# Optimization experiments

Measured on AMD Instinct MI355X. Metric: run time of the kernel, lower is better.

The kernel has to match this reference:

```python
import jax, jax.numpy as jnp
import numpy as np

NUM_ITEMS = 50000
NUM_USERS = 16384   # static number of user segments (total_user universe)
H0 = 512            # encoder_hidden_size[0]
LAT = 256           # bottleneck (encoder_hidden_size[-1] / decoder_hidden_size[0])
N = 262144          # observed interactions
NT = 262144         # target interactions


def setup_inputs() -> dict:
    key = jax.random.key(0)
    ks = jax.random.split(key, 14)

    def glorot(k, shape):
        fan_in, fan_out = shape[1], shape[0]
        lim = np.sqrt(6.0 / (fan_in + fan_out)).astype(np.float32)
        return jax.random.uniform(k, shape, jnp.float32, -lim, lim)

    return {
        "user": jax.random.randint(ks[0], (N,), 0, NUM_USERS, jnp.int32),
        "item": jax.random.randint(ks[1], (N,), 0, NUM_ITEMS, jnp.int32),
        "rating": jax.random.normal(ks[2], (N,), jnp.float32),
        "target_user": jax.random.randint(ks[3], (NT,), 0, NUM_USERS, jnp.int32),
        "target_item": jax.random.randint(ks[4], (NT,), 0, NUM_ITEMS, jnp.int32),
        "target_rating": jax.random.normal(ks[5], (NT,), jnp.float32),
        # encoder_linear: Linear(num_items, H0)
        "W_enc": glorot(ks[6], (H0, NUM_ITEMS)),
        "b_enc": jnp.zeros((H0,), jnp.float32),
        # Encoder: Linear(H0, LAT) + Tanh
        "W1": glorot(ks[7], (LAT, H0)),
        "b1": jnp.zeros((LAT,), jnp.float32),
        # Decoder: Linear(LAT, H0) + Tanh
        "W2": glorot(ks[8], (H0, LAT)),
        "b2": jnp.zeros((H0,), jnp.float32),
        # decoder_linear: Linear(H0, num_items)
        "W_dec": glorot(ks[9], (NUM_ITEMS, H0)),
        "b_dec": jnp.zeros((NUM_ITEMS,), jnp.float32),
    }


def reference(user, item, rating, target_user, target_item, target_rating,
              W_enc, b_enc, W1, b1, W2, b2, W_dec, b_dec):
    # --- encoder: gather item weight rows, scale by rating, segment-sum per user ---
    # rows: [N, H0] gather from W_enc.T ([NUM_ITEMS, H0])
    rows = W_enc.T[item] * rating[:, None]
    # per-user aggregation over the full user universe (equivalent to the
    # torch unique/sort/index_add path: users with no interactions get 0 -> tanh(bias))
    agg = jax.ops.segment_sum(rows, user, num_segments=NUM_USERS)  # [U, H0]
    x = jnp.tanh(agg + b_enc)
    # --- small dense tanh MLP encoder/decoder ---
    encoded = jnp.tanh(x @ W1.T + b1)          # [U, LAT]
    decoded = jnp.tanh(encoded @ W2.T + b2)    # [U, H0] (dropout = identity, eval mode)
    # --- decoder: gather user codes & item decoder rows, rowwise dot ---
    g = decoded[target_user]                   # [NT, H0]
    w = W_dec[target_item]                     # [NT, H0]
    pred = jnp.sum(g * w, axis=-1) + b_dec[target_item]  # [NT]
    loss = jnp.mean((pred - target_rating) ** 2)
    return pred, loss
```

## Files before the change

### kernel.cpp

```cpp
#include <hip/hip_runtime.h>
#include <hip/hip_bf16.h>
#include <math.h>

#define NUM_ITEMS 50000
#define NUM_USERS 16384
#define H0 512
#define LAT 256
#define FP8_SCALE 64.0f
#define FP8_INV (1.0f / 64.0f)

typedef __attribute__((ext_vector_type(8))) short short8;
typedef __attribute__((ext_vector_type(4))) float floatx4;
typedef __attribute__((ext_vector_type(2))) float vf2;

__device__ __forceinline__ unsigned short f2bf(float f) {
    union { float f; unsigned i; } u; u.f = f;
    unsigned r = u.i + 0x7fff + ((u.i >> 16) & 1);
    return (unsigned short)(r >> 16);
}
__device__ __forceinline__ float bfhi(unsigned v) {
    union { unsigned i; float f; } u; u.i = v & 0xffff0000u; return u.f;
}
__device__ __forceinline__ float bflo(unsigned v) {
    union { unsigned i; float f; } u; u.i = v << 16; return u.f;
}
__device__ __forceinline__ uint4 pack8(const float* v) {
    uint4 p;
    p.x = (unsigned)f2bf(v[0]) | ((unsigned)f2bf(v[1]) << 16);
    p.y = (unsigned)f2bf(v[2]) | ((unsigned)f2bf(v[3]) << 16);
    p.z = (unsigned)f2bf(v[4]) | ((unsigned)f2bf(v[5]) << 16);
    p.w = (unsigned)f2bf(v[6]) | ((unsigned)f2bf(v[7]) << 16);
    return p;
}
__device__ __forceinline__ unsigned pkfp8_4(float a, float b, float c, float d) {
    int v = __builtin_amdgcn_cvt_pk_fp8_f32(a, b, 0, false);
    v = __builtin_amdgcn_cvt_pk_fp8_f32(c, d, v, true);
    return (unsigned)v;
}
__device__ __forceinline__ void fp8x4_to_f32(unsigned v, float* o) {
    vf2 lo = __builtin_amdgcn_cvt_pk_f32_fp8((int)v, false);
    vf2 hi = __builtin_amdgcn_cvt_pk_f32_fp8((int)v, true);
    o[0] = lo.x; o[1] = lo.y; o[2] = hi.x; o[3] = hi.y;
}
__device__ __forceinline__ void unpbf8(uint4 q, float* o) {
    o[0] = bflo(q.x); o[1] = bfhi(q.x);
    o[2] = bflo(q.y); o[3] = bfhi(q.y);
    o[4] = bflo(q.z); o[5] = bfhi(q.z);
    o[6] = bflo(q.w); o[7] = bfhi(q.w);
}

__global__ __launch_bounds__(256) void count_kernel(const int* __restrict__ user, int* __restrict__ cntU,
                                                    const int* __restrict__ t_user, int* __restrict__ cntTU,
                                                    int n, int nt) {
    int i = (blockIdx.x * blockDim.x + threadIdx.x) * 4;
    if (i + 3 < n) {
        int4 u = *(const int4*)(user + i);
        atomicAdd(&cntU[u.x], 1); atomicAdd(&cntU[u.y], 1);
        atomicAdd(&cntU[u.z], 1); atomicAdd(&cntU[u.w], 1);
    } else {
        for (int k = i; k < n; ++k) atomicAdd(&cntU[user[k]], 1);
    }
    if (i + 3 < nt) {
        int4 t = *(const int4*)(t_user + i);
        atomicAdd(&cntTU[t.x], 1); atomicAdd(&cntTU[t.y], 1);
        atomicAdd(&cntTU[t.z], 1); atomicAdd(&cntTU[t.w], 1);
    } else {
        for (int k = i; k < nt; ++k) atomicAdd(&cntTU[t_user[k]], 1);
    }
}

__device__ void scan_block(const int* __restrict__ cnt, int* __restrict__ offs,
                           int* __restrict__ cursor) {
    __shared__ int wsum_s[16];
    int t = threadIdx.x;
    int lane = t & 63, wid = t >> 6;
    int base = t * 16;
    int4 a = *(const int4*)(cnt + base);
    int4 b = *(const int4*)(cnt + base + 4);
    int4 c = *(const int4*)(cnt + base + 8);
    int4 d = *(const int4*)(cnt + base + 12);
    int s = a.x + a.y + a.z + a.w + b.x + b.y + b.z + b.w
          + c.x + c.y + c.z + c.w + d.x + d.y + d.z + d.w;
    int sc = s;
#pragma unroll
    for (int off = 1; off < 64; off <<= 1) {
        int v = __shfl_up(sc, off, 64);
        if (lane >= off) sc += v;
    }
    if (lane == 63) wsum_s[wid] = sc;
    __syncthreads();
    if (t < 16) {
        int w = wsum_s[t];
        int wsc = w;
#pragma unroll
        for (int off = 1; off < 16; off <<= 1) {
            int v = __shfl_up(wsc, off, 64);
            if (t >= off) wsc += v;
        }
        wsum_s[t] = wsc - w;
    }
    __syncthreads();
    int run = wsum_s[wid] + (sc - s);
    int4 o;
    o.x = run; run += a.x; o.y = run; run += a.y; o.z = run; run += a.z; o.w = run; run += a.w;
    *(int4*)(offs + base) = o; *(int4*)(cursor + base) = o;
    o.x = run; run += b.x; o.y = run; run += b.y; o.z = run; run += b.z; o.w = run; run += b.w;
    *(int4*)(offs + base + 4) = o; *(int4*)(cursor + base + 4) = o;
    o.x = run; run += c.x; o.y = run; run += c.y; o.z = run; run += c.z; o.w = run; run += c.w;
    *(int4*)(offs + base + 8) = o; *(int4*)(cursor + base + 8) = o;
    o.x = run; run += d.x; o.y = run; run += d.y; o.z = run; run += d.z; o.w = run; run += d.w;
    *(int4*)(offs + base + 12) = o; *(int4*)(cursor + base + 12) = o;
}

__global__ void scan_kernel(const int* __restrict__ cntU, int* __restrict__ offsU, int* __restrict__ curU,
                            const int* __restrict__ cntTU, int* __restrict__ offsTU, int* __restrict__ curTU) {
    if (blockIdx.x == 0) scan_block(cntU, offsU, curU);
    else scan_block(cntTU, offsTU, curTU);
}

__global__ __launch_bounds__(256) void scatter_kernel(
        const int* __restrict__ user, const int* __restrict__ item,
        const float* __restrict__ rating, int* __restrict__ curU, int2* __restrict__ s_pack,
        const int* __restrict__ t_user, const int* __restrict__ t_item,
        const float* __restrict__ t_rating, int* __restrict__ curTU, int4* __restrict__ st_pack,
        int n, int nt) {
    int i = blockIdx.x * 256 + threadIdx.x;
    if (i < n) {
        int u = user[i];
        int pos = atomicAdd(&curU[u], 1);
        s_pack[pos] = make_int2(item[i], __float_as_int(rating[i]));
    }
    if (i < nt) {
        int tu = t_user[i];
        int pos = atomicAdd(&curTU[tu], 1);
        st_pack[pos] = make_int4(t_item[i], __float_as_int(t_rating[i]), i, 0);
    }
}

__global__ __launch_bounds__(256) void transpose_kernel(const float* __restrict__ W_enc,
                                                        unsigned char* __restrict__ wtb8) {
    __shared__ float tileh[64 * 128];
    const int TBX = (NUM_ITEMS + 127) / 128;
    int b = blockIdx.x;
    int x0 = (b % TBX) * 128;
    int y0 = (b / TBX) * 64;
    int tid = threadIdx.x;
    int g = tid >> 5;
    int m = tid & 31;
    int it4 = x0 + m * 4;
#pragma unroll
    for (int p = 0; p < 8; ++p) {
        int hloc = p * 8 + g;
        if (it4 < NUM_ITEMS) {
            float4 v = *(const float4*)(W_enc + (size_t)(y0 + hloc) * NUM_ITEMS + it4);
            *(float4*)(tileh + hloc * 128 + m * 4) = v;
        }
    }
    __syncthreads();
    int i = tid >> 1;
    int l = tid & 1;
    int it = x0 + i;
    if (it < NUM_ITEMS) {
        float f[32];
#pragma unroll
        for (int k = 0; k < 32; ++k)
            f[k] = tileh[(l * 32 + k) * 128 + i];
        uint4 o0, o1;
        o0.x = pkfp8_4(f[0] * FP8_SCALE, f[1] * FP8_SCALE, f[2] * FP8_SCALE, f[3] * FP8_SCALE);
        o0.y = pkfp8_4(f[4] * FP8_SCALE, f[5] * FP8_SCALE, f[6] * FP8_SCALE, f[7] * FP8_SCALE);
        o0.z = pkfp8_4(f[8] * FP8_SCALE, f[9] * FP8_SCALE, f[10] * FP8_SCALE, f[11] * FP8_SCALE);
        o0.w = pkfp8_4(f[12] * FP8_SCALE, f[13] * FP8_SCALE, f[14] * FP8_SCALE, f[15] * FP8_SCALE);
        o1.x = pkfp8_4(f[16] * FP8_SCALE, f[17] * FP8_SCALE, f[18] * FP8_SCALE, f[19] * FP8_SCALE);
        o1.y = pkfp8_4(f[20] * FP8_SCALE, f[21] * FP8_SCALE, f[22] * FP8_SCALE, f[23] * FP8_SCALE);
        o1.z = pkfp8_4(f[24] * FP8_SCALE, f[25] * FP8_SCALE, f[26] * FP8_SCALE, f[27] * FP8_SCALE);
        o1.w = pkfp8_4(f[28] * FP8_SCALE, f[29] * FP8_SCALE, f[30] * FP8_SCALE, f[31] * FP8_SCALE);
        unsigned char* dst = wtb8 + (size_t)it * H0 + y0 + l * 32;
        *(uint4*)dst = o0;
        *(uint4*)(dst + 16) = o1;
    }
}

__global__ __launch_bounds__(256) void cast_kernel(const float* __restrict__ W_dec,
                                                   unsigned char* __restrict__ wdb8,
                                                   const float* __restrict__ W1, unsigned short* __restrict__ w1b,
                                                   const float* __restrict__ W2, unsigned short* __restrict__ w2b,
                                                   int DB) {
    int bid = blockIdx.x;
    int tid = threadIdx.x;
    if (bid < DB) {
        size_t idx = (size_t)bid * 4096 + tid * 16;
        float4 v0 = *(const float4*)(W_dec + idx);
        float4 v1 = *(const float4*)(W_dec + idx + 4);
        float4 v2 = *(const float4*)(W_dec + idx + 8);
        float4 v3 = *(const float4*)(W_dec + idx + 12);
        uint4 o;
        o.x = pkfp8_4(v0.x * FP8_SCALE, v0.y * FP8_SCALE, v0.z * FP8_SCALE, v0.w * FP8_SCALE);
        o.y = pkfp8_4(v1.x * FP8_SCALE, v1.y * FP8_SCALE, v1.z * FP8_SCALE, v1.w * FP8_SCALE);
        o.z = pkfp8_4(v2.x * FP8_SCALE, v2.y * FP8_SCALE, v2.z * FP8_SCALE, v2.w * FP8_SCALE);
        o.w = pkfp8_4(v3.x * FP8_SCALE, v3.y * FP8_SCALE, v3.z * FP8_SCALE, v3.w * FP8_SCALE);
        *(uint4*)(wdb8 + idx) = o;
    } else {
        int b2i = bid - DB;
        const float* src = (b2i < 64) ? W1 : W2;
        unsigned short* dst = (b2i < 64) ? w1b : w2b;
        int idx = (b2i & 63) * 2048 + tid * 8;
        float v[8];
        *(float4*)&v[0] = *(const float4*)(src + idx);
        *(float4*)&v[4] = *(const float4*)(src + idx + 4);
        *(uint4*)(dst + idx) = pack8(v);
    }
}

__global__ __launch_bounds__(256) void agg_kernel(const unsigned char* __restrict__ wtb8,
                                                  const int* __restrict__ offs,
                                                  const int* __restrict__ ends,
                                                  const int2* __restrict__ s_pack,
                                                  const float* __restrict__ b_enc,
                                                  unsigned short* __restrict__ xb) {
    __shared__ float red[3 * 512];
    int u = blockIdx.x;
    int tid = threadIdx.x;
    int g = tid >> 6, lane = tid & 63;
    float acc[8] = {};
    int j0 = offs[u], j1 = ends[u];
    int j = j0 + g;
    int2 c0 = (j < j1) ? s_pack[j] : make_int2(0, 0);
    int2 c1 = (j + 4 < j1) ? s_pack[j + 4] : make_int2(0, 0);
    while (j < j1) {
        bool has1 = (j + 4) < j1;
        uint2 v0 = ((const uint2*)(wtb8 + (size_t)c0.x * H0))[lane];
        uint2 v1 = has1 ? ((const uint2*)(wtb8 + (size_t)c1.x * H0))[lane] : make_uint2(0, 0);
        int jn = j + 8;
        int2 n0 = (jn < j1) ? s_pack[jn] : make_int2(0, 0);
        int2 n1 = (jn + 4 < j1) ? s_pack[jn + 4] : make_int2(0, 0);
        float r0 = __int_as_float(c0.y);
        float wf[8];
        fp8x4_to_f32(v0.x, wf);
        fp8x4_to_f32(v0.y, wf + 4);
#pragma unroll
        for (int e = 0; e < 8; ++e) acc[e] += wf[e] * r0;
        if (has1) {
            float r1 = __int_as_float(c1.y);
            fp8x4_to_f32(v1.x, wf);
            fp8x4_to_f32(v1.y, wf + 4);
#pragma unroll
            for (int e = 0; e < 8; ++e) acc[e] += wf[e] * r1;
        }
        c0 = n0; c1 = n1; j = jn;
    }
    if (g) {
        float4* rp = (float4*)red + (size_t)(g - 1) * 128 + lane * 2;
        rp[0] = make_float4(acc[0], acc[1], acc[2], acc[3]);
        rp[1] = make_float4(acc[4], acc[5], acc[6], acc[7]);
    }
    __syncthreads();
    if (g == 0) {
#pragma unroll
        for (int h = 0; h < 3; ++h) {
            const float* rp = red + h * 512 + lane * 8;
#pragma unroll
            for (int e = 0; e < 8; ++e) acc[e] += rp[e];
        }
        float4 b0 = ((const float4*)b_enc)[lane * 2];
        float4 b1 = ((const float4*)b_enc)[lane * 2 + 1];
        float o[8];
        o[0] = tanhf(acc[0] * FP8_INV + b0.x); o[1] = tanhf(acc[1] * FP8_INV + b0.y);
        o[2] = tanhf(acc[2] * FP8_INV + b0.z); o[3] = tanhf(acc[3] * FP8_INV + b0.w);
        o[4] = tanhf(acc[4] * FP8_INV + b1.x); o[5] = tanhf(acc[5] * FP8_INV + b1.y);
        o[6] = tanhf(acc[6] * FP8_INV + b1.z); o[7] = tanhf(acc[7] * FP8_INV + b1.w);
        ((uint4*)(xb + (size_t)u * H0))[lane] = pack8(o);
    }
}

template<int BN>
__global__ __launch_bounds__(256) void gemm_mfma(const unsigned short* __restrict__ A,
                                                 const unsigned short* __restrict__ B,
                                                 const float* __restrict__ bias,
                                                 unsigned short* __restrict__ C,
                                                 int Nn, int K) {
    constexpr int WN = BN / 32;
    constexpr int NCH = 8 + BN / 16;
    constexpr int PER = NCH / 4;
    __shared__ unsigned short Ash[128 * 32];
    __shared__ unsigned short Bsh[BN * 32];
    int tid = threadIdx.x;
    int wid = tid >> 6, lane = tid & 63;
    int wave_m = wid & 1, wave_n = wid >> 1;
    int quad = lane >> 4, l16 = lane & 15;
    int m0 = blockIdx.x * 128, n0 = blockIdx.y * BN;
    floatx4 acc[4][WN] = {};
    int srow = lane >> 2;
    int scol = (lane & 3) * 8;
    for (int k0 = 0; k0 < K; k0 += 32) {
#pragma unroll
        for (int i = 0; i < PER; ++i) {
            int c = wid * PER + i;
            if (c < 8) {
                const unsigned short* ga = A + (size_t)(m0 + c * 16 + srow) * K + k0 + scol;
                __builtin_amdgcn_global_load_lds(
                    (const __attribute__((address_space(1))) void*)ga,
                    (__attribute__((address_space(3))) void*)((__attribute__((address_space(3))) char*)Ash + c * 1024),
                    16, 0, 0);
            } else {
                const unsigned short* gb = B + (size_t)(n0 + (c - 8) * 16 + srow) * K + k0 + scol;
                __builtin_amdgcn_global_load_lds(
                    (const __attribute__((address_space(1))) void*)gb,
                    (__attribute__((address_space(3))) void*)((__attribute__((address_space(3))) char*)Bsh + (c - 8) * 1024),
                    16, 0, 0);
            }
        }
        __syncthreads();
        short8 af[4], bfr[WN];
#pragma unroll
        for (int i = 0; i < 4; ++i) {
            int ml = wave_m * 64 + i * 16 + l16;
            af[i] = ((const short8*)Ash)[ml * 4 + quad];
        }
#pragma unroll
        for (int j = 0; j < WN; ++j) {
            int nl = wave_n * (BN / 2) + j * 16 + l16;
            bfr[j] = ((const short8*)Bsh)[nl * 4 + quad];
        }
#pragma unroll
        for (int i = 0; i < 4; ++i)
#pragma unroll
            for (int j = 0; j < WN; ++j)
                acc[i][j] = __builtin_amdgcn_mfma_f32_16x16x32_bf16(af[i], bfr[j], acc[i][j], 0, 0, 0);
        __syncthreads();
    }
#pragma unroll
    for (int j = 0; j < WN; ++j) {
        int col = n0 + wave_n * (BN / 2) + j * 16 + l16;
        float bv = bias[col];
#pragma unroll
        for (int i = 0; i < 4; ++i) {
            int rowb = m0 + wave_m * 64 + i * 16 + quad * 4;
#pragma unroll
            for (int r = 0; r < 4; ++r)
                C[(size_t)(rowb + r) * Nn + col] = f2bf(tanhf(acc[i][j][r] + bv));
        }
    }
}

__global__ __launch_bounds__(256) void predict_kernel(const unsigned short* __restrict__ dec_b,
                                                      const unsigned char* __restrict__ wdb8,
                                                      const float* __restrict__ b_dec,
                                                      const int* __restrict__ offs,
                                                      const int* __restrict__ ends,
                                                      const int4* __restrict__ st,
                                                      float* __restrict__ pred,
                                                      float* __restrict__ partials) {
    __shared__ float wsum[4];
    int u = blockIdx.x;
    int wid = threadIdx.x >> 6, lane = threadIdx.x & 63;
    int grp = lane >> 4, sl = lane & 15;
    int j0 = offs[u], j1 = ends[u];
    float sq = 0.f;
    if (j0 < j1) {
        const uint4* gp = (const uint4*)(dec_b + (size_t)u * H0) + sl * 4;
        float g[32];
        unpbf8(gp[0], g);
        unpbf8(gp[1], g + 8);
        unpbf8(gp[2], g + 16);
        unpbf8(gp[3], g + 24);
        for (int base = j0 + wid * 4; base < j1; base += 16) {
            int idx = base + grp;
            bool act = idx < j1;
            int4 tv = st[min(idx, j1 - 1)];
            const unsigned char* wr = wdb8 + (size_t)tv.x * H0 + sl * 32;
            uint4 wa = *(const uint4*)wr;
            uint4 wb = *(const uint4*)(wr + 16);
            unsigned wu[8] = {wa.x, wa.y, wa.z, wa.w, wb.x, wb.y, wb.z, wb.w};
            float s = 0.f;
#pragma unroll
            for (int q = 0; q < 8; ++q) {
                float wf[4];
                fp8x4_to_f32(wu[q], wf);
                s += g[q * 4 + 0] * wf[0] + g[q * 4 + 1] * wf[1]
                   + g[q * 4 + 2] * wf[2] + g[q * 4 + 3] * wf[3];
            }
            s += __shfl_xor(s, 1, 64);
            s += __shfl_xor(s, 2, 64);
            s += __shfl_xor(s, 4, 64);
            s += __shfl_xor(s, 8, 64);
            if (act && sl == 0) {
                float p = s * FP8_INV + b_dec[tv.x];
                pred[tv.z] = p;
                float d = p - __int_as_float(tv.y);
                sq += d * d;
            }
        }
    }
    sq += __shfl_xor(sq, 16, 64);
    sq += __shfl_xor(sq, 32, 64);
    if (lane == 0) wsum[wid] = sq;
    __syncthreads();
    if (threadIdx.x == 0)
        partials[u] = wsum[0] + wsum[1] + wsum[2] + wsum[3];
}

__global__ void loss_reduce(const float* __restrict__ partials, float* __restrict__ out_loss,
                            int nPart, float invNT) {
    __shared__ float s[256];
    int t = threadIdx.x;
    float a = 0.f;
    const float4* p4 = (const float4*)partials;
    int n4 = nPart >> 2;
    for (int i = t; i < n4; i += 256) {
        float4 v = p4[i];
        a += v.x + v.y + v.z + v.w;
    }
    for (int i = (n4 << 2) + t; i < nPart; i += 256) a += partials[i];
    s[t] = a;
    __syncthreads();
    for (int off = 128; off; off >>= 1) {
        if (t < off) s[t] += s[t + off];
        __syncthreads();
    }
    if (t == 0) out_loss[0] = s[0] * invNT;
}

extern "C" void kernel_launch(void* const* d_in, const int* in_sizes, int n_in,
                              void* d_out, int out_size, void* d_ws, size_t ws_size,
                              hipStream_t stream) {
    const int* user = (const int*)d_in[0];
    const int* item = (const int*)d_in[1];
    const float* rating = (const float*)d_in[2];
    const int* t_user = (const int*)d_in[3];
    const int* t_item = (const int*)d_in[4];
    const float* t_rating = (const float*)d_in[5];
    const float* W_enc = (const float*)d_in[6];
    const float* b_enc = (const float*)d_in[7];
    const float* W1 = (const float*)d_in[8];
    const float* b1 = (const float*)d_in[9];
    const float* W2 = (const float*)d_in[10];
    const float* b2 = (const float*)d_in[11];
    const float* W_dec = (const float*)d_in[12];
    const float* b_dec = (const float*)d_in[13];
    const int N = in_sizes[0];
    const int NT = in_sizes[3];

    char* ws = (char*)d_ws;
    size_t off = 0;
    auto alloc = [&](size_t bytes) {
        void* p = ws + off;
        off = (off + bytes + 255) & ~(size_t)255;
        return p;
    };
    unsigned char* wtb8 = (unsigned char*)alloc((size_t)NUM_ITEMS * H0);
    unsigned char* wdb8 = (unsigned char*)alloc((size_t)NUM_ITEMS * H0);
    unsigned short* xb = (unsigned short*)alloc((size_t)NUM_USERS * H0 * 2);
    unsigned short* enc_b = (unsigned short*)alloc((size_t)NUM_USERS * LAT * 2);
    unsigned short* dec_b = (unsigned short*)alloc((size_t)NUM_USERS * H0 * 2);
    unsigned short* w1b = (unsigned short*)alloc((size_t)LAT * H0 * 2);
    unsigned short* w2b = (unsigned short*)alloc((size_t)H0 * LAT * 2);
    int* cntU = (int*)alloc((size_t)NUM_USERS * 2 * 4);
    int* cntTU = cntU + NUM_USERS;
    int* offsU = (int*)alloc((size_t)NUM_USERS * 4);
    int* curU = (int*)alloc((size_t)NUM_USERS * 4);
    int* offsTU = (int*)alloc((size_t)NUM_USERS * 4);
    int* curTU = (int*)alloc((size_t)NUM_USERS * 4);
    int2* s_pack = (int2*)alloc((size_t)N * 8);
    int4* st_pack = (int4*)alloc((size_t)NT * 16);
    float* partials = (float*)alloc((size_t)NUM_USERS * 4);

    float* pred = (float*)d_out;
    float* loss = pred + NT;

    const int maxNNT = N > NT ? N : NT;
    const int SB = (maxNNT + 255) / 256;
    const int TBX = (NUM_ITEMS + 127) / 128;
    const int TB = TBX * (H0 / 64);
    const int DB = (NUM_ITEMS * H0) / 4096;
    const int WB = 128;

    hipMemsetAsync(cntU, 0, (size_t)NUM_USERS * 2 * 4, stream);
    count_kernel<<<(maxNNT + 1023) / 1024, 256, 0, stream>>>(user, cntU, t_user, cntTU, N, NT);
    scan_kernel<<<2, 1024, 0, stream>>>(cntU, offsU, curU, cntTU, offsTU, curTU);
    scatter_kernel<<<SB, 256, 0, stream>>>(user, item, rating, curU, s_pack,
                                           t_user, t_item, t_rating, curTU, st_pack, N, NT);
    transpose_kernel<<<TB, 256, 0, stream>>>(W_enc, wtb8);
    cast_kernel<<<DB + WB, 256, 0, stream>>>(W_dec, wdb8, W1, w1b, W2, w2b, DB);
    agg_kernel<<<NUM_USERS, 256, 0, stream>>>(wtb8, offsU, curU, s_pack, b_enc, xb);
    gemm_mfma<64><<<dim3(NUM_USERS / 128, LAT / 64), 256, 0, stream>>>(xb, w1b, b1, enc_b, LAT, H0);
    gemm_mfma<64><<<dim3(NUM_USERS / 128, H0 / 64), 256, 0, stream>>>(enc_b, w2b, b2, dec_b, H0, LAT);
    predict_kernel<<<NUM_USERS, 256, 0, stream>>>(dec_b, wdb8, b_dec, offsTU, curTU, st_pack, pred, partials);
    loss_reduce<<<1, 256, 0, stream>>>(partials, loss, NUM_USERS, 1.0f / NT);
}
```

Baseline: 416.2 us.

## Fuse preprocessing kernels and map one wavefront per user in agg and predict

Merges the scatter, W_enc transpose/fp8 quantisation and W_dec/W1/W2 cast kernels into one launch that dispatches on block index, and doubles the per-thread work in the W_dec cast. The aggregation and prediction kernels now handle one user per wavefront (four users per block) instead of one user per block. This removes the shared-memory cross-wave reduction and the block-wide sync in aggregation. Prediction now processes two targets per 16-lane group per iteration to raise memory-level parallelism. The aim is fewer launches and less idle work on users with few interactions, at the cost of more load imbalance between wavefronts and more register pressure.

```diff
diff --git a/kernel.cpp b/kernel.cpp
--- a/kernel.cpp
+++ b/kernel.cpp
@@ -118,89 +118,92 @@
     else scan_block(cntTU, offsTU, curTU);
 }
 
-__global__ __launch_bounds__(256) void scatter_kernel(
+__global__ __launch_bounds__(256) void mega_kernel(
         const int* __restrict__ user, const int* __restrict__ item,
         const float* __restrict__ rating, int* __restrict__ curU, int2* __restrict__ s_pack,
         const int* __restrict__ t_user, const int* __restrict__ t_item,
         const float* __restrict__ t_rating, int* __restrict__ curTU, int4* __restrict__ st_pack,
-        int n, int nt) {
-    int i = blockIdx.x * 256 + threadIdx.x;
-    if (i < n) {
-        int u = user[i];
-        int pos = atomicAdd(&curU[u], 1);
-        s_pack[pos] = make_int2(item[i], __float_as_int(rating[i]));
-    }
-    if (i < nt) {
-        int tu = t_user[i];
-        int pos = atomicAdd(&curTU[tu], 1);
-        st_pack[pos] = make_int4(t_item[i], __float_as_int(t_rating[i]), i, 0);
-    }
-}
-
-__global__ __launch_bounds__(256) void transpose_kernel(const float* __restrict__ W_enc,
-                                                        unsigned char* __restrict__ wtb8) {
+        const float* __restrict__ W_enc, unsigned char* __restrict__ wtb8,
+        const float* __restrict__ W_dec, unsigned char* __restrict__ wdb8,
+        const float* __restrict__ W1, unsigned short* __restrict__ w1b,
+        const float* __restrict__ W2, unsigned short* __restrict__ w2b,
+        int n, int nt, int SB, int TB, int DB) {
     __shared__ float tileh[64 * 128];
-    const int TBX = (NUM_ITEMS + 127) / 128;
-    int b = blockIdx.x;
-    int x0 = (b % TBX) * 128;
-    int y0 = (b / TBX) * 64;
-    int tid = threadIdx.x;
-    int g = tid >> 5;
-    int m = tid & 31;
-    int it4 = x0 + m * 4;
-#pragma unroll
-    for (int p = 0; p < 8; ++p) {
-        int hloc = p * 8 + g;
-        if (it4 < NUM_ITEMS) {
-            float4 v = *(const float4*)(W_enc + (size_t)(y0 + hloc) * NUM_ITEMS + it4);
-            *(float4*)(tileh + hloc * 128 + m * 4) = v;
-        }
-    }
-    __syncthreads();
-    int i = tid >> 1;
-    int l = tid & 1;
-    int it = x0 + i;
-    if (it < NUM_ITEMS) {
-        float f[32];
-#pragma unroll
-        for (int k = 0; k < 32; ++k)
-            f[k] = tileh[(l * 32 + k) * 128 + i];
-        uint4 o0, o1;
-        o0.x = pkfp8_4(f[0] * FP8_SCALE, f[1] * FP8_SCALE, f[2] * FP8_SCALE, f[3] * FP8_SCALE);
-        o0.y = pkfp8_4(f[4] * FP8_SCALE, f[5] * FP8_SCALE, f[6] * FP8_SCALE, f[7] * FP8_SCALE);
-        o0.z = pkfp8_4(f[8] * FP8_SCALE, f[9] * FP8_SCALE, f[10] * FP8_SCALE, f[11] * FP8_SCALE);
-        o0.w = pkfp8_4(f[12] * FP8_SCALE, f[13] * FP8_SCALE, f[14] * FP8_SCALE, f[15] * FP8_SCALE);
-        o1.x = pkfp8_4(f[16] * FP8_SCALE, f[17] * FP8_SCALE, f[18] * FP8_SCALE, f[19] * FP8_SCALE);
-        o1.y = pkfp8_4(f[20] * FP8_SCALE, f[21] * FP8_SCALE, f[22] * FP8_SCALE, f[23] * FP8_SCALE);
-        o1.z = pkfp8_4(f[24] * FP8_SCALE, f[25] * FP8_SCALE, f[26] * FP8_SCALE, f[27] * FP8_SCALE);
-        o1.w = pkfp8_4(f[28] * FP8_SCALE, f[29] * FP8_SCALE, f[30] * FP8_SCALE, f[31] * FP8_SCALE);
-        unsigned char* dst = wtb8 + (size_t)it * H0 + y0 + l * 32;
-        *(uint4*)dst = o0;
-        *(uint4*)(dst + 16) = o1;
-    }
-}
-
-__global__ __launch_bounds__(256) void cast_kernel(const float* __restrict__ W_dec,
-                                                   unsigned char* __restrict__ wdb8,
-                                                   const float* __restrict__ W1, unsigned short* __restrict__ w1b,
-                                                   const float* __restrict__ W2, unsigned short* __restrict__ w2b,
-                                                   int DB) {
     int bid = blockIdx.x;
     int tid = threadIdx.x;
-    if (bid < DB) {
-        size_t idx = (size_t)bid * 4096 + tid * 16;
+    if (bid < SB) {
+        int i = bid * 256 + tid;
+        if (i < n) {
+            int u = user[i];
+            int pos = atomicAdd(&curU[u], 1);
+            s_pack[pos] = make_int2(item[i], __float_as_int(rating[i]));
+        }
+        if (i < nt) {
+            int tu = t_user[i];
+            int pos = atomicAdd(&curTU[tu], 1);
+            st_pack[pos] = make_int4(t_item[i], __float_as_int(t_rating[i]), i, 0);
+        }
+    } else if (bid < SB + TB) {
+        const int TBX = (NUM_ITEMS + 127) / 128;
+        int b = bid - SB;
+        int x0 = (b % TBX) * 128;
+        int y0 = (b / TBX) * 64;
+        int g = tid >> 5;
+        int m = tid & 31;
+        int it4 = x0 + m * 4;
+#pragma unroll
+        for (int p = 0; p < 8; ++p) {
+            int hloc = p * 8 + g;
+            if (it4 < NUM_ITEMS) {
+                float4 v = *(const float4*)(W_enc + (size_t)(y0 + hloc) * NUM_ITEMS + it4);
+                *(float4*)(tileh + hloc * 128 + m * 4) = v;
+            }
+        }
+        __syncthreads();
+        int i = tid >> 1;
+        int l = tid & 1;
+        int it = x0 + i;
+        if (it < NUM_ITEMS) {
+            float f[32];
+#pragma unroll
+            for (int k = 0; k < 32; ++k)
+                f[k] = tileh[(l * 32 + k) * 128 + i];
+            uint4 o0, o1;
+            o0.x = pkfp8_4(f[0] * FP8_SCALE, f[1] * FP8_SCALE, f[2] * FP8_SCALE, f[3] * FP8_SCALE);
+            o0.y = pkfp8_4(f[4] * FP8_SCALE, f[5] * FP8_SCALE, f[6] * FP8_SCALE, f[7] * FP8_SCALE);
+            o0.z = pkfp8_4(f[8] * FP8_SCALE, f[9] * FP8_SCALE, f[10] * FP8_SCALE, f[11] * FP8_SCALE);
+            o0.w = pkfp8_4(f[12] * FP8_SCALE, f[13] * FP8_SCALE, f[14] * FP8_SCALE, f[15] * FP8_SCALE);
+            o1.x = pkfp8_4(f[16] * FP8_SCALE, f[17] * FP8_SCALE, f[18] * FP8_SCALE, f[19] * FP8_SCALE);
+            o1.y = pkfp8_4(f[20] * FP8_SCALE, f[21] * FP8_SCALE, f[22] * FP8_SCALE, f[23] * FP8_SCALE);
+            o1.z = pkfp8_4(f[24] * FP8_SCALE, f[25] * FP8_SCALE, f[26] * FP8_SCALE, f[27] * FP8_SCALE);
+            o1.w = pkfp8_4(f[28] * FP8_SCALE, f[29] * FP8_SCALE, f[30] * FP8_SCALE, f[31] * FP8_SCALE);
+            unsigned char* dst = wtb8 + (size_t)it * H0 + y0 + l * 32;
+            *(uint4*)dst = o0;
+            *(uint4*)(dst + 16) = o1;
+        }
+    } else if (bid < SB + TB + DB) {
+        size_t idx = (size_t)(bid - SB - TB) * 8192 + tid * 32;
         float4 v0 = *(const float4*)(W_dec + idx);
         float4 v1 = *(const float4*)(W_dec + idx + 4);
         float4 v2 = *(const float4*)(W_dec + idx + 8);
         float4 v3 = *(const float4*)(W_dec + idx + 12);
-        uint4 o;
-        o.x = pkfp8_4(v0.x * FP8_SCALE, v0.y * FP8_SCALE, v0.z * FP8_SCALE, v0.w * FP8_SCALE);
-        o.y = pkfp8_4(v1.x * FP8_SCALE, v1.y * FP8_SCALE, v1.z * FP8_SCALE, v1.w * FP8_SCALE);
-        o.z = pkfp8_4(v2.x * FP8_SCALE, v2.y * FP8_SCALE, v2.z * FP8_SCALE, v2.w * FP8_SCALE);
-        o.w = pkfp8_4(v3.x * FP8_SCALE, v3.y * FP8_SCALE, v3.z * FP8_SCALE, v3.w * FP8_SCALE);
-        *(uint4*)(wdb8 + idx) = o;
+        float4 v4 = *(const float4*)(W_dec + idx + 16);
+        float4 v5 = *(const float4*)(W_dec + idx + 20);
+        float4 v6 = *(const float4*)(W_dec + idx + 24);
+        float4 v7 = *(const float4*)(W_dec + idx + 28);
+        uint4 o0, o1;
+        o0.x = pkfp8_4(v0.x * FP8_SCALE, v0.y * FP8_SCALE, v0.z * FP8_SCALE, v0.w * FP8_SCALE);
+        o0.y = pkfp8_4(v1.x * FP8_SCALE, v1.y * FP8_SCALE, v1.z * FP8_SCALE, v1.w * FP8_SCALE);
+        o0.z = pkfp8_4(v2.x * FP8_SCALE, v2.y * FP8_SCALE, v2.z * FP8_SCALE, v2.w * FP8_SCALE);
+        o0.w = pkfp8_4(v3.x * FP8_SCALE, v3.y * FP8_SCALE, v3.z * FP8_SCALE, v3.w * FP8_SCALE);
+        o1.x = pkfp8_4(v4.x * FP8_SCALE, v4.y * FP8_SCALE, v4.z * FP8_SCALE, v4.w * FP8_SCALE);
+        o1.y = pkfp8_4(v5.x * FP8_SCALE, v5.y * FP8_SCALE, v5.z * FP8_SCALE, v5.w * FP8_SCALE);
+        o1.z = pkfp8_4(v6.x * FP8_SCALE, v6.y * FP8_SCALE, v6.z * FP8_SCALE, v6.w * FP8_SCALE);
+        o1.w = pkfp8_4(v7.x * FP8_SCALE, v7.y * FP8_SCALE, v7.z * FP8_SCALE, v7.w * FP8_SCALE);
+        *(uint4*)(wdb8 + idx) = o0;
+        *(uint4*)(wdb8 + idx + 16) = o1;
     } else {
-        int b2i = bid - DB;
+        int b2i = bid - SB - TB - DB;
         const float* src = (b2i < 64) ? W1 : W2;
         unsigned short* dst = (b2i < 64) ? w1b : w2b;
         int idx = (b2i & 63) * 2048 + tid * 8;
@@ -217,22 +220,20 @@
                                                   const int2* __restrict__ s_pack,
                                                   const float* __restrict__ b_enc,
                                                   unsigned short* __restrict__ xb) {
-    __shared__ float red[3 * 512];
-    int u = blockIdx.x;
-    int tid = threadIdx.x;
-    int g = tid >> 6, lane = tid & 63;
+    int wid = threadIdx.x >> 6, lane = threadIdx.x & 63;
+    int u = blockIdx.x * 4 + wid;
+    int j0 = offs[u], j1 = ends[u];
     float acc[8] = {};
-    int j0 = offs[u], j1 = ends[u];
-    int j = j0 + g;
+    int j = j0;
     int2 c0 = (j < j1) ? s_pack[j] : make_int2(0, 0);
-    int2 c1 = (j + 4 < j1) ? s_pack[j + 4] : make_int2(0, 0);
+    int2 c1 = (j + 1 < j1) ? s_pack[j + 1] : make_int2(0, 0);
     while (j < j1) {
-        bool has1 = (j + 4) < j1;
+        bool has1 = (j + 1) < j1;
         uint2 v0 = ((const uint2*)(wtb8 + (size_t)c0.x * H0))[lane];
         uint2 v1 = has1 ? ((const uint2*)(wtb8 + (size_t)c1.x * H0))[lane] : make_uint2(0, 0);
-        int jn = j + 8;
+        int jn = j + 2;
         int2 n0 = (jn < j1) ? s_pack[jn] : make_int2(0, 0);
-        int2 n1 = (jn + 4 < j1) ? s_pack[jn + 4] : make_int2(0, 0);
+        int2 n1 = (jn + 1 < j1) ? s_pack[jn + 1] : make_int2(0, 0);
         float r0 = __int_as_float(c0.y);
         float wf[8];
         fp8x4_to_f32(v0.x, wf);
@@ -248,28 +249,14 @@
         }
         c0 = n0; c1 = n1; j = jn;
     }
-    if (g) {
-        float4* rp = (float4*)red + (size_t)(g - 1) * 128 + lane * 2;
-        rp[0] = make_float4(acc[0], acc[1], acc[2], acc[3]);
-        rp[1] = make_float4(acc[4], acc[5], acc[6], acc[7]);
-    }
-    __syncthreads();
-    if (g == 0) {
-#pragma unroll
-        for (int h = 0; h < 3; ++h) {
-            const float* rp = red + h * 512 + lane * 8;
-#pragma unroll
-            for (int e = 0; e < 8; ++e) acc[e] += rp[e];
-        }
-        float4 b0 = ((const float4*)b_enc)[lane * 2];
-        float4 b1 = ((const float4*)b_enc)[lane * 2 + 1];
-        float o[8];
-        o[0] = tanhf(acc[0] * FP8_INV + b0.x); o[1] = tanhf(acc[1] * FP8_INV + b0.y);
-        o[2] = tanhf(acc[2] * FP8_INV + b0.z); o[3] = tanhf(acc[3] * FP8_INV + b0.w);
-        o[4] = tanhf(acc[4] * FP8_INV + b1.x); o[5] = tanhf(acc[5] * FP8_INV + b1.y);
-        o[6] = tanhf(acc[6] * FP8_INV + b1.z); o[7] = tanhf(acc[7] * FP8_INV + b1.w);
-        ((uint4*)(xb + (size_t)u * H0))[lane] = pack8(o);
-    }
+    float4 b0 = ((const float4*)b_enc)[lane * 2];
+    float4 b1 = ((const float4*)b_enc)[lane * 2 + 1];
+    float o[8];
+    o[0] = tanhf(acc[0] * FP8_INV + b0.x); o[1] = tanhf(acc[1] * FP8_INV + b0.y);
+    o[2] = tanhf(acc[2] * FP8_INV + b0.z); o[3] = tanhf(acc[3] * FP8_INV + b0.w);
+    o[4] = tanhf(acc[4] * FP8_INV + b1.x); o[5] = tanhf(acc[5] * FP8_INV + b1.y);
+    o[6] = tanhf(acc[6] * FP8_INV + b1.z); o[7] = tanhf(acc[7] * FP8_INV + b1.w);
+    ((uint4*)(xb + (size_t)u * H0))[lane] = pack8(o);
 }
 
 template<int BN>
@@ -351,9 +338,9 @@
                                                       float* __restrict__ pred,
                                                       float* __restrict__ partials) {
     __shared__ float wsum[4];
-    int u = blockIdx.x;
     int wid = threadIdx.x >> 6, lane = threadIdx.x & 63;
     int grp = lane >> 4, sl = lane & 15;
+    int u = blockIdx.x * 4 + wid;
     int j0 = offs[u], j1 = ends[u];
     float sq = 0.f;
     if (j0 < j1) {
@@ -363,31 +350,48 @@
         unpbf8(gp[1], g + 8);
         unpbf8(gp[2], g + 16);
         unpbf8(gp[3], g + 24);
-        for (int base = j0 + wid * 4; base < j1; base += 16) {
-            int idx = base + grp;
-            bool act = idx < j1;
-            int4 tv = st[min(idx, j1 - 1)];
-            const unsigned char* wr = wdb8 + (size_t)tv.x * H0 + sl * 32;
-            uint4 wa = *(const uint4*)wr;
-            uint4 wb = *(const uint4*)(wr + 16);
-            unsigned wu[8] = {wa.x, wa.y, wa.z, wa.w, wb.x, wb.y, wb.z, wb.w};
-            float s = 0.f;
+        for (int base = j0; base < j1; base += 8) {
+            int i0 = base + grp, i1 = base + 4 + grp;
+            bool a0 = i0 < j1, a1 = i1 < j1;
+            int4 t0 = st[min(i0, j1 - 1)];
+            int4 t1 = st[min(i1, j1 - 1)];
+            const unsigned char* w0p = wdb8 + (size_t)t0.x * H0 + sl * 32;
+            const unsigned char* w1p = wdb8 + (size_t)t1.x * H0 + sl * 32;
+            uint4 wa0 = *(const uint4*)w0p;
+            uint4 wb0 = *(const uint4*)(w0p + 16);
+            uint4 wa1 = *(const uint4*)w1p;
+            uint4 wb1 = *(const uint4*)(w1p + 16);
+            unsigned wu0[8] = {wa0.x, wa0.y, wa0.z, wa0.w, wb0.x, wb0.y, wb0.z, wb0.w};
+            unsigned wu1[8] = {wa1.x, wa1.y, wa1.z, wa1.w, wb1.x, wb1.y, wb1.z, wb1.w};
+            float s0 = 0.f, s1 = 0.f;
 #pragma unroll
             for (int q = 0; q < 8; ++q) {
                 float wf[4];
-                fp8x4_to_f32(wu[q], wf);
-                s += g[q * 4 + 0] * wf[0] + g[q * 4 + 1] * wf[1]
-                   + g[q * 4 + 2] * wf[2] + g[q * 4 + 3] * wf[3];
+                fp8x4_to_f32(wu0[q], wf);
+                s0 += g[q * 4 + 0] * wf[0] + g[q * 4 + 1] * wf[1]
+                    + g[q * 4 + 2] * wf[2] + g[q * 4 + 3] * wf[3];
+                fp8x4_to_f32(wu1[q], wf);
+                s1 += g[q * 4 + 0] * wf[0] + g[q * 4 + 1] * wf[1]
+                    + g[q * 4 + 2] * wf[2] + g[q * 4 + 3] * wf[3];
             }
-            s += __shfl_xor(s, 1, 64);
-            s += __shfl_xor(s, 2, 64);
-            s += __shfl_xor(s, 4, 64);
-            s += __shfl_xor(s, 8, 64);
-            if (act && sl == 0) {
-                float p = s * FP8_INV + b_dec[tv.x];
-                pred[tv.z] = p;
-                float d = p - __int_as_float(tv.y);
-                sq += d * d;
+#pragma unroll
+            for (int off = 1; off < 16; off <<= 1) {
+                s0 += __shfl_xor(s0, off, 64);
+                s1 += __shfl_xor(s1, off, 64);
+            }
+            if (sl == 0) {
+                if (a0) {
+                    float p = s0 * FP8_INV + b_dec[t0.x];
+                    pred[t0.z] = p;
+                    float d = p - __int_as_float(t0.y);
+                    sq += d * d;
+                }
+                if (a1) {
+                    float p = s1 * FP8_INV + b_dec[t1.x];
+                    pred[t1.z] = p;
+                    float d = p - __int_as_float(t1.y);
+                    sq += d * d;
+                }
             }
         }
     }
@@ -396,7 +400,7 @@
     if (lane == 0) wsum[wid] = sq;
     __syncthreads();
     if (threadIdx.x == 0)
-        partials[u] = wsum[0] + wsum[1] + wsum[2] + wsum[3];
+        partials[blockIdx.x] = wsum[0] + wsum[1] + wsum[2] + wsum[3];
 }
 
 __global__ void loss_reduce(const float* __restrict__ partials, float* __restrict__ out_loss,
@@ -462,7 +466,7 @@
     int* curTU = (int*)alloc((size_t)NUM_USERS * 4);
     int2* s_pack = (int2*)alloc((size_t)N * 8);
     int4* st_pack = (int4*)alloc((size_t)NT * 16);
-    float* partials = (float*)alloc((size_t)NUM_USERS * 4);
+    float* partials = (float*)alloc((size_t)(NUM_USERS / 4) * 4);
 
     float* pred = (float*)d_out;
     float* loss = pred + NT;
@@ -471,19 +475,20 @@
     const int SB = (maxNNT + 255) / 256;
     const int TBX = (NUM_ITEMS + 127) / 128;
     const int TB = TBX * (H0 / 64);
-    const int DB = (NUM_ITEMS * H0) / 4096;
+    const int DB = (NUM_ITEMS * H0) / 8192;
     const int WB = 128;
 
     hipMemsetAsync(cntU, 0, (size_t)NUM_USERS * 2 * 4, stream);
     count_kernel<<<(maxNNT + 1023) / 1024, 256, 0, stream>>>(user, cntU, t_user, cntTU, N, NT);
     scan_kernel<<<2, 1024, 0, stream>>>(cntU, offsU, curU, cntTU, offsTU, curTU);
-    scatter_kernel<<<SB, 256, 0, stream>>>(user, item, rating, curU, s_pack,
-                                           t_user, t_item, t_rating, curTU, st_pack, N, NT);
-    transpose_kernel<<<TB, 256, 0, stream>>>(W_enc, wtb8);
-    cast_kernel<<<DB + WB, 256, 0, stream>>>(W_dec, wdb8, W1, w1b, W2, w2b, DB);
-    agg_kernel<<<NUM_USERS, 256, 0, stream>>>(wtb8, offsU, curU, s_pack, b_enc, xb);
+    mega_kernel<<<SB + TB + DB + WB, 256, 0, stream>>>(
+        user, item, rating, curU, s_pack,
+        t_user, t_item, t_rating, curTU, st_pack,
+        W_enc, wtb8, W_dec, wdb8, W1, w1b, W2, w2b,
+        N, NT, SB, TB, DB);
+    agg_kernel<<<NUM_USERS / 4, 256, 0, stream>>>(wtb8, offsU, curU, s_pack, b_enc, xb);
     gemm_mfma<64><<<dim3(NUM_USERS / 128, LAT / 64), 256, 0, stream>>>(xb, w1b, b1, enc_b, LAT, H0);
     gemm_mfma<64><<<dim3(NUM_USERS / 128, H0 / 64), 256, 0, stream>>>(enc_b, w2b, b2, dec_b, H0, LAT);
-    predict_kernel<<<NUM_USERS, 256, 0, stream>>>(dec_b, wdb8, b_dec, offsTU, curTU, st_pack, pred, partials);
-    loss_reduce<<<1, 256, 0, stream>>>(partials, loss, NUM_USERS, 1.0f / NT);
-}
+    predict_kernel<<<NUM_USERS / 4, 256, 0, stream>>>(dec_b, wdb8, b_dec, offsTU, curTU, st_pack, pred, partials);
+    loss_reduce<<<1, 256, 0, stream>>>(partials, loss, NUM_USERS / 4, 1.0f / NT);
+}
```

Measured after the change: 400.3 us. -3.8%, faster.
